# Performance work log

Hardware: AMD Instinct MI355X
Metric: run time of the kernel (lower is better)

The kernel has to match this reference:

```python
import jax, jax.numpy as jnp
import numpy as np

N_GRAPHS = 500
NODES_PER_GRAPH = 200
EDGES_PER_GRAPH = 6400
N = N_GRAPHS * NODES_PER_GRAPH          # 100000 nodes
E = N_GRAPHS * EDGES_PER_GRAPH          # 3200000 edges
D = 256                                  # dim_hidden
RATIO = 0.8
EPS = 1e-12


def setup_inputs() -> dict:
    key = jax.random.key(0)
    k1, k2 = jax.random.split(key, 2)
    x = jax.random.normal(k1, (N, D), dtype=jnp.float32)
    # edges consistent with batch: both endpoints inside the same graph
    rng = np.random.default_rng(0)
    g = np.repeat(np.arange(N_GRAPHS, dtype=np.int32), EDGES_PER_GRAPH)
    row = g * NODES_PER_GRAPH + rng.integers(0, NODES_PER_GRAPH, E).astype(np.int32)
    col = g * NODES_PER_GRAPH + rng.integers(0, NODES_PER_GRAPH, E).astype(np.int32)
    edge_index = jnp.asarray(np.stack([row, col]), dtype=jnp.int32)
    batch = jnp.asarray(np.repeat(np.arange(N_GRAPHS, dtype=np.int32), NODES_PER_GRAPH))
    W = jax.random.normal(k2, (2 * D, 1), dtype=jnp.float32) * (1.0 / np.sqrt(2 * D))
    b = jnp.zeros((1,), dtype=jnp.float32)
    return {"x": x, "edge_index": edge_index, "batch": batch, "W": W, "b": b}


def _edge_scores(x, W, b, edge_index):
    # concat(x[row], x[col]) @ W == (x @ W_row)[row] + (x @ W_col)[col]
    # -> avoids materializing the [E, 2D] edge_rep tensor.
    row, col = edge_index[0], edge_index[1]
    s_row = x @ W[:D, 0]   # [N]
    s_col = x @ W[D:, 0]   # [N]
    return s_row[row] + s_col[col] + b[0]  # [E]


def _topk_edge_mask(edge_score, edge_graph):
    # sparse_sort (descending=True): norm = minmax(score) - graph_id; argsort desc.
    f_min, f_max = edge_score.min(), edge_score.max()
    norm = (edge_score - f_min) / (f_max - f_min + EPS) - edge_graph.astype(edge_score.dtype)
    perm = jnp.argsort(-norm)  # graphs ascending, score descending within graph
    deg = jax.ops.segment_sum(jnp.ones_like(edge_graph), edge_graph, num_segments=N_GRAPHS)
    k = jnp.ceil(RATIO * deg.astype(jnp.float32)).astype(deg.dtype)
    start = jnp.concatenate([jnp.zeros((1,), deg.dtype), jnp.cumsum(deg)[:-1]])
    sg = edge_graph[perm]                        # graph id in sorted order
    pos = jnp.arange(E, dtype=deg.dtype) - start[sg]  # rank within segment
    keep_sorted = pos < k[sg]
    # scatter keep flags back to original edge order
    return jnp.zeros((E,), dtype=bool).at[perm].set(keep_sorted)


def _relabel(x, batch, edge_index, emask):
    # padded equivalent of torch.unique + scatter relabel:
    # selected nodes are compacted to the front of x/batch; dropped slots -> -1.
    row, col = edge_index[0], edge_index[1]
    m = emask.astype(jnp.int32)
    sel = (jnp.zeros((N,), jnp.int32).at[row].max(m).at[col].max(m)).astype(bool)
    new_id = jnp.where(sel, jnp.cumsum(sel) - 1, -1)           # [N]
    new_ei = jnp.where(emask[None, :], new_id[edge_index], -1)  # [2, E], -1 = padding
    order = jnp.argsort(~sel)                                   # stable: selected first
    x_out = x[order]                                            # [N, D], selected at front
    batch_out = jnp.where(sel[order], batch[order], -1)
    return x_out, new_ei, batch_out, sel.sum()


def reference(x, edge_index, batch, W, b):
    edge_score = _edge_scores(x, W, b, edge_index)
    edge_graph = batch[edge_index[0]]
    mask = _topk_edge_mask(edge_score, edge_graph)   # True = causal edge
    causal_w = jnp.where(mask, edge_score, 0.0)
    conf_w = jnp.where(mask, 0.0, -edge_score)
    causal_x, causal_ei, causal_batch, n_causal = _relabel(x, batch, edge_index, mask)
    conf_x, conf_ei, conf_batch, n_conf = _relabel(x, batch, edge_index, ~mask)
    return (causal_x, causal_ei, causal_w, causal_batch, n_causal,
            conf_x, conf_ei, conf_w, conf_batch, n_conf,
            edge_score, mask)
```

## Files before the change

kernel.cpp:

```cpp
#include <hip/hip_runtime.h>
#include <cmath>

typedef unsigned long long u64;
typedef unsigned int u32;
typedef unsigned char u8;

#define DHID 256
#define NMAX 100000
#define EMAX 3200000
#define EPGMAX 6400
#define NBLKMAX 128
#define TOPK_T 512

__device__ float g_srow[NMAX];
__device__ float g_scol[NMAX];
__device__ float g_escore[EMAX];
__device__ int   g_destC[NMAX];
__device__ int   g_destF[NMAX];
__device__ int   g_invC[NMAX];
__device__ int   g_invF[NMAX];
__device__ u8    g_selC[NMAX];
__device__ u8    g_selF[NMAX];
__device__ u8    g_mask[EMAX];
__device__ float g_pmin[1024];
__device__ float g_pmax[1024];
__device__ int   g_blkC[NBLKMAX];
__device__ int   g_blkF[NBLKMAX];
__device__ int   g_tot[2];

__global__ void k_node_scores(const float* __restrict__ x, const float* __restrict__ W, int N){
  int t = blockIdx.x*256 + threadIdx.x;
  if (t < N){ g_selC[t] = 0; g_selF[t] = 0; }
  int lane = threadIdx.x & 63, wave = threadIdx.x >> 6;
  int n = blockIdx.x*4 + wave;
  if (n >= N) return;
  float4 xv = ((const float4*)(x + (size_t)n*DHID))[lane];
  float4 wr = ((const float4*)W)[lane];
  float4 wc = ((const float4*)W)[64 + lane];
  double dr = (double)xv.x*wr.x + (double)xv.y*wr.y + (double)xv.z*wr.z + (double)xv.w*wr.w;
  double dc = (double)xv.x*wc.x + (double)xv.y*wc.y + (double)xv.z*wc.z + (double)xv.w*wc.w;
  #pragma unroll
  for (int off = 32; off; off >>= 1){
    dr += __shfl_xor(dr, off);
    dc += __shfl_xor(dc, off);
  }
  if (lane == 0){ g_srow[n] = (float)dr; g_scol[n] = (float)dc; }
}

__global__ void k_minmax_part(const int* __restrict__ ei, const float* __restrict__ b, int E){
  float b0 = b[0];
  float lmin = INFINITY, lmax = -INFINITY;
  for (int e = blockIdx.x*256 + threadIdx.x; e < E; e += gridDim.x*256){
    int r = ei[e], c = ei[E + e];
    float s = (g_srow[r] + g_scol[c]) + b0;
    g_escore[e] = s;
    lmin = fminf(lmin, s); lmax = fmaxf(lmax, s);
  }
  #pragma unroll
  for (int off = 32; off; off >>= 1){
    lmin = fminf(lmin, __shfl_xor(lmin, off));
    lmax = fmaxf(lmax, __shfl_xor(lmax, off));
  }
  __shared__ float smin[4], smax[4];
  int lane = threadIdx.x & 63, wid = threadIdx.x >> 6;
  if (lane == 0){ smin[wid] = lmin; smax[wid] = lmax; }
  __syncthreads();
  if (threadIdx.x == 0){
    float m0 = fminf(fminf(smin[0], smin[1]), fminf(smin[2], smin[3]));
    float m1 = fmaxf(fmaxf(smax[0], smax[1]), fmaxf(smax[2], smax[3]));
    g_pmin[blockIdx.x] = m0; g_pmax[blockIdx.x] = m1;
  }
}

__global__ __launch_bounds__(TOPK_T) void k_topk(const int* __restrict__ ei,
    float* __restrict__ out, long long oCW, long long oFW, long long oS, long long oM,
    int E, int EPG, int k){
  __shared__ u32 keys[EPGMAX];
  __shared__ u8  keep[EPGMAX];
  __shared__ int hist[256];
  __shared__ float wred[8], wred2[8];
  __shared__ int wsum[8];
  __shared__ u32 sh_prefix;
  __shared__ int sh_rem, sh_rem_next, sh_digit;
  int g = blockIdx.x, tid = threadIdx.x;
  int lane = tid & 63, wid = tid >> 6;
  long long base = (long long)g * EPG;

  float lmin = fminf(g_pmin[tid], g_pmin[tid + 512]);
  float lmax = fmaxf(g_pmax[tid], g_pmax[tid + 512]);
  #pragma unroll
  for (int off = 32; off; off >>= 1){
    lmin = fminf(lmin, __shfl_xor(lmin, off));
    lmax = fmaxf(lmax, __shfl_xor(lmax, off));
  }
  if (lane == 0){ wred[wid] = lmin; wred2[wid] = lmax; }
  if (tid == 0){ sh_prefix = 0; sh_rem = k; }
  __syncthreads();
  float fmin = wred[0], fmax = wred2[0];
  #pragma unroll
  for (int w = 1; w < 8; w++){
    fmin = fminf(fmin, wred[w]); fmax = fmaxf(fmax, wred2[w]);
  }

  float denom = (fmax - fmin) + 1e-12f;
  float gf = (float)g;

  for (int i = tid; i < EPG; i += TOPK_T){
    float s = g_escore[base + i];
    float frac = (s - fmin) / denom;
    float nk = frac - gf;
    u32 u = __float_as_uint(nk);
    u = (u & 0x80000000u) ? ~u : (u | 0x80000000u);
    keys[i] = ~u;
  }
  for (int shift = 24; shift >= 0; shift -= 8){
    if (tid < 256) hist[tid] = 0;
    __syncthreads();
    u32 pref = sh_prefix;
    for (int i = tid; i < EPG; i += TOPK_T){
      u32 kk = keys[i];
      bool cand = (shift == 24) || ((kk >> (shift + 8)) == pref);
      if (cand){
        u32 digit = (kk >> shift) & 0xFF;
        u32 d0 = __builtin_amdgcn_readfirstlane(digit);
        if (__all(digit == d0)){
          u64 m = __ballot(1);
          if (lane == __builtin_ctzll(m)) atomicAdd(&hist[d0], (int)__popcll(m));
        } else {
          atomicAdd(&hist[digit], 1);
        }
      }
    }
    __syncthreads();
    int v = 0, inc = 0;
    if (tid < 256){
      v = hist[tid];
      inc = v;
      #pragma unroll
      for (int off = 1; off < 64; off <<= 1){
        int t2 = __shfl_up(inc, off);
        if (lane >= off) inc += t2;
      }
      if (lane == 63) wsum[wid] = inc;
    }
    __syncthreads();
    if (tid < 256){
      int wpre = 0;
      for (int w = 0; w < wid; w++) wpre += wsum[w];
      int incl = inc + wpre;
      int cumprev = incl - v;
      int rem = sh_rem;
      if (cumprev < rem && rem <= incl){
        sh_digit = tid;
        sh_rem_next = rem - cumprev;
      }
    }
    __syncthreads();
    if (tid == 0){
      sh_prefix = (sh_prefix << 8) | (u32)sh_digit;
      sh_rem = sh_rem_next;
    }
    __syncthreads();
  }
  u32 T = sh_prefix;
  int r_budget = sh_rem;

  int CH = (EPG + TOPK_T - 1) / TOPK_T;
  int c0 = tid * CH;
  int cnt = 0;
  for (int j = 0; j < CH; j++){
    int i = c0 + j;
    if (i < EPG && keys[i] == T) cnt++;
  }
  int inc2 = cnt;
  #pragma unroll
  for (int off = 1; off < 64; off <<= 1){
    int t2 = __shfl_up(inc2, off);
    if (lane >= off) inc2 += t2;
  }
  if (lane == 63) wsum[wid] = inc2;
  __syncthreads();
  int wpre2 = 0;
  for (int w = 0; w < wid; w++) wpre2 += wsum[w];
  int rank = inc2 - cnt + wpre2;

  for (int j = 0; j < CH; j++){
    int i = c0 + j;
    if (i >= EPG) break;
    u32 kk = keys[i];
    int kept;
    if (kk < T) kept = 1;
    else if (kk == T){ kept = (rank < r_budget); rank++; }
    else kept = 0;
    keep[i] = (u8)kept;
  }
  __syncthreads();

  for (int i = tid; i < EPG; i += TOPK_T){
    long long e = base + i;
    int kept = keep[i];
    float s = g_escore[e];
    int rr = ei[e], cc = ei[E + e];
    g_mask[e] = (u8)kept;
    out[oS + e]  = s;
    out[oM + e]  = kept ? 1.0f : 0.0f;
    out[oCW + e] = kept ? s : 0.0f;
    out[oFW + e] = kept ? 0.0f : -s;
    if (kept){ g_selC[rr] = 1; g_selC[cc] = 1; }
    else     { g_selF[rr] = 1; g_selF[cc] = 1; }
  }
}

__global__ void k_blocksum(int N){
  int bb = blockIdx.x, tid = threadIdx.x;
  int start = bb*1024;
  int c = 0, f = 0;
  #pragma unroll
  for (int q = 0; q < 4; q++){
    int n = start + tid*4 + q;
    if (n < N){ c += g_selC[n]; f += g_selF[n]; }
  }
  #pragma unroll
  for (int off = 32; off; off >>= 1){
    c += __shfl_xor(c, off); f += __shfl_xor(f, off);
  }
  __shared__ int sc[4], sf[4];
  int lane = tid & 63, wid = tid >> 6;
  if (lane == 0){ sc[wid] = c; sf[wid] = f; }
  __syncthreads();
  if (tid == 0){
    g_blkC[bb] = sc[0]+sc[1]+sc[2]+sc[3];
    g_blkF[bb] = sf[0]+sf[1]+sf[2]+sf[3];
  }
}

__global__ void k_scanblk(int nb, float* __restrict__ out, long long oNC, long long oNF){
  __shared__ int wsC[2], wsF[2];
  int tid = threadIdx.x;
  int lane = tid & 63, wid = tid >> 6;
  int c = (tid < nb) ? g_blkC[tid] : 0;
  int f = (tid < nb) ? g_blkF[tid] : 0;
  int ic = c, iff = f;
  #pragma unroll
  for (int off = 1; off < 64; off <<= 1){
    int a = __shfl_up(ic, off), b2 = __shfl_up(iff, off);
    if (lane >= off){ ic += a; iff += b2; }
  }
  if (lane == 63){ wsC[wid] = ic; wsF[wid] = iff; }
  __syncthreads();
  int pc = (wid == 1) ? wsC[0] : 0;
  int pf = (wid == 1) ? wsF[0] : 0;
  if (tid < nb){ g_blkC[tid] = ic - c + pc; g_blkF[tid] = iff - f + pf; }
  if (tid == NBLKMAX - 1){
    g_tot[0] = ic + pc; g_tot[1] = iff + pf;
    out[oNC] = (float)(ic + pc);
    out[oNF] = (float)(iff + pf);
  }
}

__global__ void k_dest(const int* __restrict__ batch,
    float* __restrict__ out, long long oCB, long long oFB, int N){
  int bb = blockIdx.x, tid = threadIdx.x;
  int start = bb*1024;
  int idx0 = start + tid*4;
  int c[4], f[4]; int sc = 0, sf = 0;
  #pragma unroll
  for (int q = 0; q < 4; q++){
    int n = idx0 + q;
    int vc = (n < N) ? (int)g_selC[n] : 0;
    int vf = (n < N) ? (int)g_selF[n] : 0;
    c[q] = vc; f[q] = vf; sc += vc; sf += vf;
  }
  int lane = tid & 63, wid = tid >> 6;
  int ic = sc, iff = sf;
  #pragma unroll
  for (int off = 1; off < 64; off <<= 1){
    int a = __shfl_up(ic, off), b2 = __shfl_up(iff, off);
    if (lane >= off){ ic += a; iff += b2; }
  }
  __shared__ int wsC[4], wsF[4];
  if (lane == 63){ wsC[wid] = ic; wsF[wid] = iff; }
  __syncthreads();
  int wpreC = 0, wpreF = 0;
  for (int w = 0; w < wid; w++){ wpreC += wsC[w]; wpreF += wsF[w]; }
  int excC = (ic - sc + wpreC) + g_blkC[bb];
  int excF = (iff - sf + wpreF) + g_blkF[bb];
  int nC = g_tot[0], nF = g_tot[1];
  int runC = 0, runF = 0;
  #pragma unroll
  for (int q = 0; q < 4; q++){
    int n = idx0 + q;
    if (n >= N) break;
    runC += c[q]; runF += f[q];
    int cumC = excC + runC;
    int cumF = excF + runF;
    int dC = c[q] ? (cumC - 1) : (nC + (n - cumC));
    int dF = f[q] ? (cumF - 1) : (nF + (n - cumF));
    dC = min(max(dC, 0), N-1);
    dF = min(max(dF, 0), N-1);
    g_destC[n] = dC; g_destF[n] = dF;
    g_invC[dC] = n; g_invF[dF] = n;
    float bt = (float)batch[n];
    out[oCB + dC] = c[q] ? bt : -1.0f;
    out[oFB + dF] = f[q] ? bt : -1.0f;
  }
}

__global__ void k_out(const int* __restrict__ ei, const float* __restrict__ x,
    float* __restrict__ out, long long oCE, long long oFE,
    long long oCX, long long oFX, int E, int N, int EB){
  int bid = blockIdx.x, tid = threadIdx.x;
  if (bid < EB){
    int e = bid*256 + tid;
    if (e >= E) return;
    int r = ei[e], c = ei[E + e];
    int m = g_mask[e];
    out[oCE + e]     = m ? (float)g_destC[r] : -1.0f;
    out[oCE + E + e] = m ? (float)g_destC[c] : -1.0f;
    out[oFE + e]     = m ? -1.0f : (float)g_destF[r];
    out[oFE + E + e] = m ? -1.0f : (float)g_destF[c];
    return;
  }
  int row = (bid - EB)*4 + (tid >> 6);
  int cq  = tid & 63;
  if (row < N){
    int src = g_invC[row];
    float4 v = ((const float4*)(x + (size_t)src*DHID))[cq];
    *reinterpret_cast<float4*>(out + oCX + (long long)row*DHID + cq*4) = v;
  } else if (row < 2*N){
    int m = row - N;
    int src = g_invF[m];
    float4 v = ((const float4*)(x + (size_t)src*DHID))[cq];
    long long iF = oFX + (long long)m*DHID + cq*4;
    out[iF] = v.x;
    float2 mid; mid.x = v.y; mid.y = v.z;
    *reinterpret_cast<float2*>(out + iF + 1) = mid;
    out[iF + 3] = v.w;
  }
}

extern "C" void kernel_launch(void* const* d_in, const int* in_sizes, int n_in,
                              void* d_out, int out_size, void* d_ws, size_t ws_size,
                              hipStream_t stream) {
  const float* x   = (const float*)d_in[0];
  const int* ei    = (const int*)d_in[1];
  const int* batch = (const int*)d_in[2];
  const float* W   = (const float*)d_in[3];
  const float* b   = (const float*)d_in[4];
  float* out = (float*)d_out;

  int N   = in_sizes[0] / DHID;
  int E   = in_sizes[1] / 2;
  if (N > NMAX) N = NMAX;
  if (E > EMAX) E = EMAX;
  const int G   = N / 200;
  int EPG = (G > 0) ? E / G : 0;
  if (EPG > EPGMAX) EPG = EPGMAX;
  const int k   = (int)ceilf(0.8f * (float)EPG);

  long long oCX = 0;
  long long oCE = oCX + (long long)N*DHID;
  long long oCW = oCE + 2LL*E;
  long long oCB = oCW + E;
  long long oNC = oCB + N;
  long long oFX = oNC + 1;
  long long oFE = oFX + (long long)N*DHID;
  long long oFW = oFE + 2LL*E;
  long long oFB = oFW + E;
  long long oNF = oFB + N;
  long long oS  = oNF + 1;
  long long oM  = oS + E;

  k_node_scores<<<(N + 3)/4, 256, 0, stream>>>(x, W, N);
  k_minmax_part<<<1024, 256, 0, stream>>>(ei, b, E);
  k_topk<<<G, TOPK_T, 0, stream>>>(ei, out, oCW, oFW, oS, oM, E, EPG, k);
  int nblk = (N + 1023)/1024;
  k_blocksum<<<nblk, 256, 0, stream>>>(N);
  k_scanblk<<<1, NBLKMAX, 0, stream>>>(nblk, out, oNC, oNF);
  k_dest<<<nblk, 256, 0, stream>>>(batch, out, oCB, oFB, N);
  int EB = (E + 255)/256;
  int XB = (2*N + 3)/4;
  k_out<<<EB + XB, 256, 0, stream>>>(ei, x, out, oCE, oFE, oCX, oFX, E, N, EB);
}
```

Before: 173.3 us.

## Fuse node scoring and edge scoring per graph using shared-memory node scores

Merges the node-score and edge-score/minmax kernels into one kernel with one block per graph. Each block computes its 200 node scores into shared memory and then gathers from LDS instead of global arrays. The score output write moves here out of topk, and topk is widened to 1024 threads. This relies on the fixed 200 nodes and 6400 edges per graph layout and clamps the local indices. Only 500 blocks now do the node dot products, which may reduce parallelism for the x read.

```diff
diff --git a/kernel.cpp b/kernel.cpp
--- a/kernel.cpp
+++ b/kernel.cpp
@@ -9,11 +9,10 @@
 #define NMAX 100000
 #define EMAX 3200000
 #define EPGMAX 6400
+#define NPG 200
 #define NBLKMAX 128
-#define TOPK_T 512
-
-__device__ float g_srow[NMAX];
-__device__ float g_scol[NMAX];
+#define TOPK_T 1024
+
 __device__ float g_escore[EMAX];
 __device__ int   g_destC[NMAX];
 __device__ int   g_destF[NMAX];
@@ -22,38 +21,52 @@
 __device__ u8    g_selC[NMAX];
 __device__ u8    g_selF[NMAX];
 __device__ u8    g_mask[EMAX];
-__device__ float g_pmin[1024];
-__device__ float g_pmax[1024];
+__device__ float g_pmin[512];
+__device__ float g_pmax[512];
 __device__ int   g_blkC[NBLKMAX];
 __device__ int   g_blkF[NBLKMAX];
 __device__ int   g_tot[2];
 
-__global__ void k_node_scores(const float* __restrict__ x, const float* __restrict__ W, int N){
-  int t = blockIdx.x*256 + threadIdx.x;
-  if (t < N){ g_selC[t] = 0; g_selF[t] = 0; }
-  int lane = threadIdx.x & 63, wave = threadIdx.x >> 6;
-  int n = blockIdx.x*4 + wave;
-  if (n >= N) return;
-  float4 xv = ((const float4*)(x + (size_t)n*DHID))[lane];
+__global__ __launch_bounds__(256) void k_scores_full(const float* __restrict__ x,
+    const int* __restrict__ ei, const float* __restrict__ W, const float* __restrict__ b,
+    float* __restrict__ out, long long oS, int E, int N){
+  __shared__ float srow_l[NPG], scol_l[NPG];
+  __shared__ float smin[4], smax[4];
+  int g = blockIdx.x, tid = threadIdx.x;
+  int lane = tid & 63, wid = tid >> 6;
+  int nbase = g * NPG;
+
+  if (tid < NPG){ g_selC[nbase + tid] = 0; g_selF[nbase + tid] = 0; }
+
   float4 wr = ((const float4*)W)[lane];
   float4 wc = ((const float4*)W)[64 + lane];
-  double dr = (double)xv.x*wr.x + (double)xv.y*wr.y + (double)xv.z*wr.z + (double)xv.w*wr.w;
-  double dc = (double)xv.x*wc.x + (double)xv.y*wc.y + (double)xv.z*wc.z + (double)xv.w*wc.w;
-  #pragma unroll
-  for (int off = 32; off; off >>= 1){
-    dr += __shfl_xor(dr, off);
-    dc += __shfl_xor(dc, off);
-  }
-  if (lane == 0){ g_srow[n] = (float)dr; g_scol[n] = (float)dc; }
-}
-
-__global__ void k_minmax_part(const int* __restrict__ ei, const float* __restrict__ b, int E){
+  for (int it = 0; it < NPG/4; it++){
+    int n0 = it*4 + wid;
+    int n = nbase + n0;
+    float4 xv = ((const float4*)(x + (size_t)n*DHID))[lane];
+    double dr = (double)xv.x*wr.x + (double)xv.y*wr.y + (double)xv.z*wr.z + (double)xv.w*wr.w;
+    double dc = (double)xv.x*wc.x + (double)xv.y*wc.y + (double)xv.z*wc.z + (double)xv.w*wc.w;
+    #pragma unroll
+    for (int off = 32; off; off >>= 1){
+      dr += __shfl_xor(dr, off);
+      dc += __shfl_xor(dc, off);
+    }
+    if (lane == 0){ srow_l[n0] = (float)dr; scol_l[n0] = (float)dc; }
+  }
+  __syncthreads();
+
   float b0 = b[0];
   float lmin = INFINITY, lmax = -INFINITY;
-  for (int e = blockIdx.x*256 + threadIdx.x; e < E; e += gridDim.x*256){
-    int r = ei[e], c = ei[E + e];
-    float s = (g_srow[r] + g_scol[c]) + b0;
+  long long ebase = (long long)g * EPGMAX;
+  for (int it = 0; it < EPGMAX/256; it++){
+    long long e = ebase + it*256 + tid;
+    int r0 = ei[e]     - nbase;
+    int c0 = ei[E + e] - nbase;
+    r0 = min(max(r0, 0), NPG-1);
+    c0 = min(max(c0, 0), NPG-1);
+    float s = (srow_l[r0] + scol_l[c0]) + b0;
     g_escore[e] = s;
+    out[oS + e] = s;
     lmin = fminf(lmin, s); lmax = fmaxf(lmax, s);
   }
   #pragma unroll
@@ -61,33 +74,31 @@
     lmin = fminf(lmin, __shfl_xor(lmin, off));
     lmax = fmaxf(lmax, __shfl_xor(lmax, off));
   }
-  __shared__ float smin[4], smax[4];
-  int lane = threadIdx.x & 63, wid = threadIdx.x >> 6;
   if (lane == 0){ smin[wid] = lmin; smax[wid] = lmax; }
   __syncthreads();
-  if (threadIdx.x == 0){
-    float m0 = fminf(fminf(smin[0], smin[1]), fminf(smin[2], smin[3]));
-    float m1 = fmaxf(fmaxf(smax[0], smax[1]), fmaxf(smax[2], smax[3]));
-    g_pmin[blockIdx.x] = m0; g_pmax[blockIdx.x] = m1;
+  if (tid == 0){
+    g_pmin[g] = fminf(fminf(smin[0], smin[1]), fminf(smin[2], smin[3]));
+    g_pmax[g] = fmaxf(fmaxf(smax[0], smax[1]), fmaxf(smax[2], smax[3]));
   }
 }
 
 __global__ __launch_bounds__(TOPK_T) void k_topk(const int* __restrict__ ei,
-    float* __restrict__ out, long long oCW, long long oFW, long long oS, long long oM,
+    float* __restrict__ out, long long oCW, long long oFW, long long oM,
     int E, int EPG, int k){
   __shared__ u32 keys[EPGMAX];
   __shared__ u8  keep[EPGMAX];
   __shared__ int hist[256];
-  __shared__ float wred[8], wred2[8];
-  __shared__ int wsum[8];
+  __shared__ float wred[16], wred2[16];
+  __shared__ int wsum[16];
   __shared__ u32 sh_prefix;
   __shared__ int sh_rem, sh_rem_next, sh_digit;
   int g = blockIdx.x, tid = threadIdx.x;
   int lane = tid & 63, wid = tid >> 6;
+  int G = (int)gridDim.x;
   long long base = (long long)g * EPG;
 
-  float lmin = fminf(g_pmin[tid], g_pmin[tid + 512]);
-  float lmax = fmaxf(g_pmax[tid], g_pmax[tid + 512]);
+  float lmin = (tid < G) ? g_pmin[tid] : INFINITY;
+  float lmax = (tid < G) ? g_pmax[tid] : -INFINITY;
   #pragma unroll
   for (int off = 32; off; off >>= 1){
     lmin = fminf(lmin, __shfl_xor(lmin, off));
@@ -98,7 +109,7 @@
   __syncthreads();
   float fmin = wred[0], fmax = wred2[0];
   #pragma unroll
-  for (int w = 1; w < 8; w++){
+  for (int w = 1; w < 16; w++){
     fmin = fminf(fmin, wred[w]); fmax = fmaxf(fmax, wred2[w]);
   }
 
@@ -202,7 +213,6 @@
     float s = g_escore[e];
     int rr = ei[e], cc = ei[E + e];
     g_mask[e] = (u8)kept;
-    out[oS + e]  = s;
     out[oM + e]  = kept ? 1.0f : 0.0f;
     out[oCW + e] = kept ? s : 0.0f;
     out[oFW + e] = kept ? 0.0f : -s;
@@ -353,7 +363,7 @@
   int E   = in_sizes[1] / 2;
   if (N > NMAX) N = NMAX;
   if (E > EMAX) E = EMAX;
-  const int G   = N / 200;
+  const int G   = N / NPG;
   int EPG = (G > 0) ? E / G : 0;
   if (EPG > EPGMAX) EPG = EPGMAX;
   const int k   = (int)ceilf(0.8f * (float)EPG);
@@ -371,9 +381,8 @@
   long long oS  = oNF + 1;
   long long oM  = oS + E;
 
-  k_node_scores<<<(N + 3)/4, 256, 0, stream>>>(x, W, N);
-  k_minmax_part<<<1024, 256, 0, stream>>>(ei, b, E);
-  k_topk<<<G, TOPK_T, 0, stream>>>(ei, out, oCW, oFW, oS, oM, E, EPG, k);
+  k_scores_full<<<G, 256, 0, stream>>>(x, ei, W, b, out, oS, E, N);
+  k_topk<<<G, TOPK_T, 0, stream>>>(ei, out, oCW, oFW, oM, E, EPG, k);
   int nblk = (N + 1023)/1024;
   k_blocksum<<<nblk, 256, 0, stream>>>(N);
   k_scanblk<<<1, NBLKMAX, 0, stream>>>(nblk, out, oNC, oNF);
```

Result: no change. 171.0 us (-1.4%).
